# Kernel tuning notes

Hardware: AMD Instinct MI355X
Metric: run time of the kernel (lower is better)

The kernel has to match this reference:

```python
import jax, jax.numpy as jnp
import numpy as np

B, N, C, H = 4, 4096, 512, 16  # batch, seq (=input_resolution), dim, num_heads


def setup_inputs() -> dict:
    key = jax.random.key(0)
    k1, k2, k3, k4 = jax.random.split(key, 4)
    x = jax.random.normal(k1, (B, N, C), jnp.float32)
    Wqk = jax.random.normal(k2, (C, 2 * C), jnp.float32) / np.sqrt(C)
    bqk = jnp.zeros((2 * C,), jnp.float32)
    lepe_w = jax.random.normal(k3, (C, 1, 3), jnp.float32) * 0.1  # depthwise conv, groups=C
    lepe_b = jnp.zeros((C,), jnp.float32)
    return {"x": x, "Wqk": Wqk, "bqk": bqk, "lepe_w": lepe_w, "lepe_b": lepe_b}


def _rope(x):
    # x: [b, n, c]; 1D RoPE over the sequence axis, k_max = c // 2 pairs.
    b, n, c = x.shape
    k_max = c // 2
    theta = 1.0 / (10000.0 ** (jnp.arange(k_max, dtype=jnp.float32) / k_max))
    ang = jnp.arange(n, dtype=jnp.float32)[:, None] * theta  # [n, k_max]
    cos, sin = jnp.cos(ang), jnp.sin(ang)
    xr, xi = x[..., 0::2], x[..., 1::2]  # consecutive (re, im) pairs
    out = jnp.stack([xr * cos - xi * sin, xr * sin + xi * cos], axis=-1)
    return out.reshape(b, n, c)


def reference(x, Wqk, bqk, lepe_w, lepe_b):
    b, n, c = x.shape
    h = H
    d = c // h
    qk = x @ Wqk + bqk  # [b, n, 2c]
    q = jax.nn.elu(qk[..., :c]) + 1.0
    k = jax.nn.elu(qk[..., c:]) + 1.0
    q_rope = _rope(q).reshape(b, n, h, d).transpose(0, 2, 1, 3)  # [b,h,n,d]
    k_rope = _rope(k).reshape(b, n, h, d).transpose(0, 2, 1, 3)
    qh = q.reshape(b, n, h, d).transpose(0, 2, 1, 3)
    kh = k.reshape(b, n, h, d).transpose(0, 2, 1, 3)
    v = x.reshape(b, n, h, d).transpose(0, 2, 1, 3)
    # normalizer z = 1 / (q . mean_n(k) + eps)
    kmean = kh.mean(axis=2)  # [b,h,d]
    z = 1.0 / (jnp.einsum('bhnd,bhd->bhn', qh, kmean) + 1e-6)  # [b,h,n]
    # kv = (k_rope^T / sqrt(n)) @ (v / sqrt(n))
    kv = jnp.einsum('bhnd,bhne->bhde', k_rope, v) / n  # [b,h,d,d]
    out = jnp.einsum('bhnd,bhde->bhne', q_rope, kv) * z[..., None]  # [b,h,n,d]
    out = out.transpose(0, 2, 1, 3).reshape(b, n, c)
    # LePE: depthwise conv1d over sequence on v (v reassembled == x)
    vt = x.transpose(0, 2, 1)  # [b, c, n]
    lepe = jax.lax.conv_general_dilated(
        vt, lepe_w, window_strides=(1,), padding=((1, 1),),
        feature_group_count=c, dimension_numbers=('NCH', 'OIH', 'NCH'))
    lepe = lepe + lepe_b[None, :, None]
    return out + lepe.transpose(0, 2, 1)
```

## Files before the change

kernel.cpp:

```cpp
#include <hip/hip_runtime.h>

typedef unsigned short u16;
typedef u16   u16x8 __attribute__((ext_vector_type(8)));
typedef short s16x8 __attribute__((ext_vector_type(8)));
typedef float f32x4 __attribute__((ext_vector_type(4)));

__device__ __forceinline__ float b2f(u16 u) {
    return __uint_as_float(((unsigned)u) << 16);
}
__device__ __forceinline__ u16 f2b(float f) {
    unsigned x = __float_as_uint(f);
    x += 0x7fffu + ((x >> 16) & 1u);
    return (u16)(x >> 16);
}
__device__ __forceinline__ void gload_lds(const u16* g, u16* l) {
    __builtin_amdgcn_global_load_lds(
        (const __attribute__((address_space(1))) unsigned int*)g,
        (__attribute__((address_space(3))) unsigned int*)l, 16, 0, 0);
}

#define THETA_SCALE 0.05190512648261f

__global__ __launch_bounds__(256)
void k_prep(const float* __restrict__ X, u16* __restrict__ Xb,
            const float* __restrict__ W, u16* __restrict__ WT) {
    if (blockIdx.x < 4096) {
        size_t i = (size_t)(blockIdx.x * 256 + threadIdx.x) * 8;
        float4 a = *(const float4*)(X + i);
        float4 b = *(const float4*)(X + i + 4);
        u16x8 r;
        r[0] = f2b(a.x); r[1] = f2b(a.y); r[2] = f2b(a.z); r[3] = f2b(a.w);
        r[4] = f2b(b.x); r[5] = f2b(b.y); r[6] = f2b(b.z); r[7] = f2b(b.w);
        *(u16x8*)(Xb + i) = r;
    } else {
        __shared__ float tile[32][33];
        int bid = blockIdx.x - 4096;
        int c0 = (bid & 31) * 32;
        int r0 = (bid >> 5) * 32;
        int tx = threadIdx.x & 31;
        int ty = threadIdx.x >> 5;
        #pragma unroll
        for (int i = 0; i < 4; ++i) {
            int r = ty + i * 8;
            tile[r][tx] = W[(size_t)(r0 + r) * 1024 + c0 + tx];
        }
        __syncthreads();
        #pragma unroll
        for (int i = 0; i < 4; ++i) {
            int r = ty + i * 8;
            WT[(size_t)(c0 + r) * 512 + r0 + tx] = f2b(tile[tx][r]);
        }
    }
}

__global__ __launch_bounds__(256)
void k_gemm(const u16* __restrict__ Xb, const u16* __restrict__ WT,
            const float* __restrict__ bqk,
            u16* __restrict__ Qb, u16* __restrict__ Kb) {
    __shared__ u16 As[128 * 64];
    __shared__ u16 Bs[128 * 64];
    const int t = threadIdx.x;
    const int m0 = blockIdx.x * 128;
    const int n0 = blockIdx.y * 128;
    const int lane = t & 63;
    const int wave = t >> 6;
    const int wm = (wave >> 1) * 64;
    const int wn = (wave & 1) * 64;
    const int quad = lane >> 4;
    const int l16 = lane & 15;
    const int lr = lane >> 3;
    const int cg = ((lane & 7) ^ lr) * 8;

    f32x4 acc[4][4];
    f32x4 zero4 = {0.f, 0.f, 0.f, 0.f};
    #pragma unroll
    for (int i = 0; i < 4; ++i)
        #pragma unroll
        for (int j = 0; j < 4; ++j) acc[i][j] = zero4;

    for (int k0 = 0; k0 < 512; k0 += 64) {
        __syncthreads();
        #pragma unroll
        for (int g = 0; g < 4; ++g) {
            int r0 = wave * 32 + g * 8;
            size_t ga = (size_t)(m0 + r0 + lr) * 512 + k0 + cg;
            size_t gb = (size_t)(n0 + r0 + lr) * 512 + k0 + cg;
            gload_lds(Xb + ga, &As[r0 * 64]);
            gload_lds(WT + gb, &Bs[r0 * 64]);
        }
        __syncthreads();
        #pragma unroll
        for (int ks = 0; ks < 64; ks += 32) {
            const int cbase = quad + (ks >> 3);
            s16x8 a4[4], b4[4];
            #pragma unroll
            for (int i = 0; i < 4; ++i) {
                int row = wm + i * 16 + l16;
                a4[i] = *(const s16x8*)&As[row * 64 + ((cbase ^ (row & 7)) * 8)];
            }
            #pragma unroll
            for (int j = 0; j < 4; ++j) {
                int row = wn + j * 16 + l16;
                b4[j] = *(const s16x8*)&Bs[row * 64 + ((cbase ^ (row & 7)) * 8)];
            }
            #pragma unroll
            for (int i = 0; i < 4; ++i)
                #pragma unroll
                for (int j = 0; j < 4; ++j)
                    acc[i][j] = __builtin_amdgcn_mfma_f32_16x16x32_bf16(
                        a4[i], b4[j], acc[i][j], 0, 0, 0);
        }
    }

    u16* O = (n0 < 512) ? Qb : Kb;
    #pragma unroll
    for (int i = 0; i < 4; ++i)
        #pragma unroll
        for (int j = 0; j < 4; ++j) {
            int col = n0 + wn + j * 16 + l16;
            float bias = bqk[col];
            int gc = col & 511;
            #pragma unroll
            for (int r = 0; r < 4; ++r) {
                int grow = m0 + wm + i * 16 + quad * 4 + r;
                float v = acc[i][j][r] + bias;
                v = v > 0.f ? v + 1.f : __expf(v);
                O[(size_t)grow * 512 + gc] = f2b(v);
            }
        }
}

__global__ __launch_bounds__(256)
void k_kv(const u16* __restrict__ Kb, const u16* __restrict__ Xb,
          float* __restrict__ kvbuf, float* __restrict__ ksum) {
    const int bh = blockIdx.x;
    const int b = bh >> 4, h = bh & 15;
    const int nb = blockIdx.y * 512;
    __shared__ float krT_s[32 * 68];
    __shared__ float v_s[64 * 36];
    __shared__ float red_s[256 * 16];
    const int t = threadIdx.x;
    const int row = t >> 2;
    const int c8 = (t & 3) * 8;
    const int d0 = (t & 15) * 2;
    const int e0 = ((t >> 4) & 3) * 8;
    const int rg = (t >> 6) * 16;
    float ksl[8] = {0, 0, 0, 0, 0, 0, 0, 0};
    float a0[8] = {0, 0, 0, 0, 0, 0, 0, 0};
    float a1[8] = {0, 0, 0, 0, 0, 0, 0, 0};

    float th[4];
    #pragma unroll
    for (int p = 0; p < 4; ++p)
        th[p] = exp2f(-THETA_SCALE * (float)(h * 16 + (c8 >> 1) + p));

    for (int pass = 0; pass < 8; ++pass) {
        int n = nb + pass * 64 + row;
        size_t base = (size_t)(b * 4096 + n) * 512 + h * 32 + c8;
        u16x8 k8 = *(const u16x8*)(Kb + base);
        u16x8 v8 = *(const u16x8*)(Xb + base);
        float kf[8], vf[8], kr[8];
        #pragma unroll
        for (int j = 0; j < 8; ++j) { kf[j] = b2f(k8[j]); vf[j] = b2f(v8[j]); }
        #pragma unroll
        for (int p = 0; p < 4; ++p) {
            float sv, cv;
            sincosf((float)n * th[p], &sv, &cv);
            kr[2 * p]     = kf[2 * p] * cv - kf[2 * p + 1] * sv;
            kr[2 * p + 1] = kf[2 * p] * sv + kf[2 * p + 1] * cv;
        }
        #pragma unroll
        for (int j = 0; j < 8; ++j) ksl[j] += kf[j];
        if (pass) __syncthreads();
        #pragma unroll
        for (int j = 0; j < 8; ++j) krT_s[(c8 + j) * 68 + row] = kr[j];
        *(float4*)&v_s[row * 36 + c8]     = make_float4(vf[0], vf[1], vf[2], vf[3]);
        *(float4*)&v_s[row * 36 + c8 + 4] = make_float4(vf[4], vf[5], vf[6], vf[7]);
        __syncthreads();
        #pragma unroll
        for (int r = 0; r < 16; r += 4) {
            int rr0 = rg + r;
            float4 k0 = *(const float4*)&krT_s[d0 * 68 + rr0];
            float4 k1 = *(const float4*)&krT_s[(d0 + 1) * 68 + rr0];
            #pragma unroll
            for (int rr = 0; rr < 4; ++rr) {
                float4 va = *(const float4*)&v_s[(rr0 + rr) * 36 + e0];
                float4 vb = *(const float4*)&v_s[(rr0 + rr) * 36 + e0 + 4];
                float kq0 = (rr == 0) ? k0.x : (rr == 1) ? k0.y : (rr == 2) ? k0.z : k0.w;
                float kq1 = (rr == 0) ? k1.x : (rr == 1) ? k1.y : (rr == 2) ? k1.z : k1.w;
                a0[0] += kq0 * va.x; a0[1] += kq0 * va.y; a0[2] += kq0 * va.z; a0[3] += kq0 * va.w;
                a0[4] += kq0 * vb.x; a0[5] += kq0 * vb.y; a0[6] += kq0 * vb.z; a0[7] += kq0 * vb.w;
                a1[0] += kq1 * va.x; a1[1] += kq1 * va.y; a1[2] += kq1 * va.z; a1[3] += kq1 * va.w;
                a1[4] += kq1 * vb.x; a1[5] += kq1 * vb.y; a1[6] += kq1 * vb.z; a1[7] += kq1 * vb.w;
            }
        }
    }
    __syncthreads();
    #pragma unroll
    for (int j = 0; j < 8; ++j) {
        red_s[t * 16 + j] = a0[j];
        red_s[t * 16 + 8 + j] = a1[j];
    }
    __syncthreads();
    if (t < 64) {
        #pragma unroll
        for (int i = 0; i < 16; ++i) {
            float s = red_s[t * 16 + i] + red_s[(t + 64) * 16 + i] +
                      red_s[(t + 128) * 16 + i] + red_s[(t + 192) * 16 + i];
            int dd = (t & 15) * 2 + (i >> 3);
            int ee = ((t >> 4) & 3) * 8 + (i & 7);
            atomicAdd(&kvbuf[(size_t)bh * 1024 + dd * 32 + ee], s);
        }
    }
    __syncthreads();
    #pragma unroll
    for (int j = 0; j < 8; ++j) red_s[row * 32 + c8 + j] = ksl[j];
    __syncthreads();
    if (t < 32) {
        float s = 0.f;
        for (int r = 0; r < 64; ++r) s += red_s[r * 32 + t];
        atomicAdd(&ksum[bh * 32 + t], s);
    }
}

__global__ __launch_bounds__(256)
void k_out(const u16* __restrict__ Qb, const u16* __restrict__ Xb,
           const float* __restrict__ kvbuf, const float* __restrict__ ksum,
           const float* __restrict__ lw, const float* __restrict__ lb,
           float* __restrict__ OUT) {
    const int b = blockIdx.x >> 6;
    const int nb = (blockIdx.x & 63) * 64;
    const int hbase = blockIdx.y * 4;
    __shared__ float kv_s[32 * 36];
    __shared__ float qr_s[64 * 36];
    __shared__ float ks_s[32];
    __shared__ float z_s[64];
    const int t = threadIdx.x;
    const int row = t >> 2;
    const int c4 = t & 3;
    const int e0 = c4 * 8;
    const float invN = 1.f / 4096.f;
    const int n = nb + row;
    const size_t rowbase = (size_t)(b * 4096 + n) * 512;

    for (int hh = 0; hh < 4; ++hh) {
        const int h = hbase + hh;
        const int bh = b * 16 + h;
        if (hh) __syncthreads();
        #pragma unroll
        for (int i = 0; i < 4; ++i) {
            int id = t + i * 256;
            kv_s[(id >> 5) * 36 + (id & 31)] = kvbuf[(size_t)bh * 1024 + id] * invN;
        }
        if (t < 32) ks_s[t] = ksum[bh * 32 + t] * invN;
        __syncthreads();

        u16x8 q8 = *(const u16x8*)(Qb + rowbase + h * 32 + e0);
        float qf[8];
        #pragma unroll
        for (int j = 0; j < 8; ++j) qf[j] = b2f(q8[j]);
        float part = 0.f;
        #pragma unroll
        for (int j = 0; j < 8; ++j) part += qf[j] * ks_s[e0 + j];
        float qr[8];
        #pragma unroll
        for (int p = 0; p < 4; ++p) {
            float th = exp2f(-THETA_SCALE * (float)(h * 16 + c4 * 4 + p));
            float sv, cv;
            sincosf((float)n * th, &sv, &cv);
            qr[2 * p]     = qf[2 * p] * cv - qf[2 * p + 1] * sv;
            qr[2 * p + 1] = qf[2 * p] * sv + qf[2 * p + 1] * cv;
        }
        *(float4*)&qr_s[row * 36 + e0]     = make_float4(qr[0], qr[1], qr[2], qr[3]);
        *(float4*)&qr_s[row * 36 + e0 + 4] = make_float4(qr[4], qr[5], qr[6], qr[7]);
        part += __shfl_xor(part, 1);
        part += __shfl_xor(part, 2);
        if (c4 == 0) z_s[row] = 1.f / (part + 1e-6f);
        __syncthreads();

        float o[8] = {0, 0, 0, 0, 0, 0, 0, 0};
        #pragma unroll 4
        for (int dd = 0; dd < 32; ++dd) {
            float qd = qr_s[row * 36 + dd];
            const float4 k0v = *(const float4*)&kv_s[dd * 36 + e0];
            const float4 k1v = *(const float4*)&kv_s[dd * 36 + e0 + 4];
            o[0] += qd * k0v.x; o[1] += qd * k0v.y; o[2] += qd * k0v.z; o[3] += qd * k0v.w;
            o[4] += qd * k1v.x; o[5] += qd * k1v.y; o[6] += qd * k1v.z; o[7] += qd * k1v.w;
        }
        const float z = z_s[row];

        const int cb = h * 32 + e0;
        u16x8 xc = *(const u16x8*)(Xb + rowbase + cb);
        u16x8 xm = {0, 0, 0, 0, 0, 0, 0, 0};
        u16x8 xp = {0, 0, 0, 0, 0, 0, 0, 0};
        if (n > 0)    xm = *(const u16x8*)(Xb + rowbase - 512 + cb);
        if (n < 4095) xp = *(const u16x8*)(Xb + rowbase + 512 + cb);
        float rv[8];
        #pragma unroll
        for (int j = 0; j < 8; ++j) {
            int c = cb + j;
            float lep = b2f(xm[j]) * lw[c * 3] +
                        b2f(xc[j]) * lw[c * 3 + 1] +
                        b2f(xp[j]) * lw[c * 3 + 2] + lb[c];
            rv[j] = o[j] * z + lep;
        }
        float* Of = OUT + rowbase + cb;
        *(float4*)Of       = make_float4(rv[0], rv[1], rv[2], rv[3]);
        *(float4*)(Of + 4) = make_float4(rv[4], rv[5], rv[6], rv[7]);
    }
}

extern "C" void kernel_launch(void* const* d_in, const int* in_sizes, int n_in,
                              void* d_out, int out_size, void* d_ws, size_t ws_size,
                              hipStream_t stream) {
    const float* x   = (const float*)d_in[0];
    const float* Wqk = (const float*)d_in[1];
    const float* bqk = (const float*)d_in[2];
    const float* lw  = (const float*)d_in[3];
    const float* lb  = (const float*)d_in[4];
    float* out = (float*)d_out;

    char* w = (char*)d_ws;
    u16* Kb      = (u16*)w;   w += (size_t)16384 * 512 * 2;
    u16* Qb      = (u16*)w;   w += (size_t)16384 * 512 * 2;
    u16* Xb      = (u16*)w;   w += (size_t)16384 * 512 * 2;
    u16* WT      = (u16*)w;   w += (size_t)1024 * 512 * 2;
    float* kvbuf = (float*)w; w += (size_t)64 * 1024 * 4;
    float* ksum  = (float*)w;

    hipMemsetAsync(kvbuf, 0, (size_t)64 * 1024 * 4 + (size_t)64 * 32 * 4, stream);
    k_prep<<<4608, 256, 0, stream>>>(x, Xb, Wqk, WT);
    k_gemm<<<dim3(128, 8), 256, 0, stream>>>(Xb, WT, bqk, Qb, Kb);
    k_kv<<<dim3(64, 8), 256, 0, stream>>>(Kb, Xb, kvbuf, ksum);
    k_out<<<dim3(256, 4), 256, 0, stream>>>(Qb, Xb, kvbuf, ksum, lw, lb, out);
}
```

Measured before the change: 168.4 us.

## Use bf16 MFMA for kv accumulation and fold buffer zeroing into prep kernel

The k_v/k_rope outer-product reduction now stages rotated K and V transposed in swizzled bf16 LDS tiles and accumulates with 16x16x32 bf16 MFMA instructions. This replaces the scalar FP32 FMA loop and the shared-memory cross-thread reduction. The separate memset of the kv and ksum accumulators is replaced by extra blocks in the prep kernel, saving one launch. Rounding rotated K to bf16 adds some precision loss.

```diff
diff --git a/kernel.cpp b/kernel.cpp
--- a/kernel.cpp
+++ b/kernel.cpp
@@ -23,7 +23,8 @@
 
 __global__ __launch_bounds__(256)
 void k_prep(const float* __restrict__ X, u16* __restrict__ Xb,
-            const float* __restrict__ W, u16* __restrict__ WT) {
+            const float* __restrict__ W, u16* __restrict__ WT,
+            float* __restrict__ kvz) {
     if (blockIdx.x < 4096) {
         size_t i = (size_t)(blockIdx.x * 256 + threadIdx.x) * 8;
         float4 a = *(const float4*)(X + i);
@@ -32,7 +33,7 @@
         r[0] = f2b(a.x); r[1] = f2b(a.y); r[2] = f2b(a.z); r[3] = f2b(a.w);
         r[4] = f2b(b.x); r[5] = f2b(b.y); r[6] = f2b(b.z); r[7] = f2b(b.w);
         *(u16x8*)(Xb + i) = r;
-    } else {
+    } else if (blockIdx.x < 4608) {
         __shared__ float tile[32][33];
         int bid = blockIdx.x - 4096;
         int c0 = (bid & 31) * 32;
@@ -50,6 +51,9 @@
             int r = ty + i * 8;
             WT[(size_t)(c0 + r) * 512 + r0 + tx] = f2b(tile[tx][r]);
         }
+    } else {
+        size_t i = (size_t)(blockIdx.x - 4608) * 1024 + threadIdx.x * 4;
+        *(float4*)(kvz + i) = make_float4(0.f, 0.f, 0.f, 0.f);
     }
 }
 
@@ -136,18 +140,26 @@
     const int bh = blockIdx.x;
     const int b = bh >> 4, h = bh & 15;
     const int nb = blockIdx.y * 512;
-    __shared__ float krT_s[32 * 68];
-    __shared__ float v_s[64 * 36];
-    __shared__ float red_s[256 * 16];
+    __shared__ u16 krT[32 * 72];
+    __shared__ u16 vT[32 * 72];
+    __shared__ float red[64 * 36];
     const int t = threadIdx.x;
     const int row = t >> 2;
     const int c8 = (t & 3) * 8;
-    const int d0 = (t & 15) * 2;
-    const int e0 = ((t >> 4) & 3) * 8;
-    const int rg = (t >> 6) * 16;
+    const int rot_w = 16 * ((c8 >> 3) & 3);
+    const int lane = t & 63;
+    const int wave = t >> 6;
+    const int quad = lane >> 4;
+    const int l16 = lane & 15;
+    const int dq = (wave >> 1) * 16;
+    const int eq = (wave & 1) * 16;
+    const int ca = dq + l16;
+    const int cb2 = eq + l16;
+    const int rot_a = 16 * ((ca >> 3) & 3);
+    const int rot_b = 16 * ((cb2 >> 3) & 3);
+
     float ksl[8] = {0, 0, 0, 0, 0, 0, 0, 0};
-    float a0[8] = {0, 0, 0, 0, 0, 0, 0, 0};
-    float a1[8] = {0, 0, 0, 0, 0, 0, 0, 0};
+    f32x4 acc = {0.f, 0.f, 0.f, 0.f};
 
     float th[4];
     #pragma unroll
@@ -159,9 +171,9 @@
         size_t base = (size_t)(b * 4096 + n) * 512 + h * 32 + c8;
         u16x8 k8 = *(const u16x8*)(Kb + base);
         u16x8 v8 = *(const u16x8*)(Xb + base);
-        float kf[8], vf[8], kr[8];
-        #pragma unroll
-        for (int j = 0; j < 8; ++j) { kf[j] = b2f(k8[j]); vf[j] = b2f(v8[j]); }
+        float kf[8], kr[8];
+        #pragma unroll
+        for (int j = 0; j < 8; ++j) kf[j] = b2f(k8[j]);
         #pragma unroll
         for (int p = 0; p < 4; ++p) {
             float sv, cv;
@@ -172,53 +184,33 @@
         #pragma unroll
         for (int j = 0; j < 8; ++j) ksl[j] += kf[j];
         if (pass) __syncthreads();
-        #pragma unroll
-        for (int j = 0; j < 8; ++j) krT_s[(c8 + j) * 68 + row] = kr[j];
-        *(float4*)&v_s[row * 36 + c8]     = make_float4(vf[0], vf[1], vf[2], vf[3]);
-        *(float4*)&v_s[row * 36 + c8 + 4] = make_float4(vf[4], vf[5], vf[6], vf[7]);
-        __syncthreads();
-        #pragma unroll
-        for (int r = 0; r < 16; r += 4) {
-            int rr0 = rg + r;
-            float4 k0 = *(const float4*)&krT_s[d0 * 68 + rr0];
-            float4 k1 = *(const float4*)&krT_s[(d0 + 1) * 68 + rr0];
-            #pragma unroll
-            for (int rr = 0; rr < 4; ++rr) {
-                float4 va = *(const float4*)&v_s[(rr0 + rr) * 36 + e0];
-                float4 vb = *(const float4*)&v_s[(rr0 + rr) * 36 + e0 + 4];
-                float kq0 = (rr == 0) ? k0.x : (rr == 1) ? k0.y : (rr == 2) ? k0.z : k0.w;
-                float kq1 = (rr == 0) ? k1.x : (rr == 1) ? k1.y : (rr == 2) ? k1.z : k1.w;
-                a0[0] += kq0 * va.x; a0[1] += kq0 * va.y; a0[2] += kq0 * va.z; a0[3] += kq0 * va.w;
-                a0[4] += kq0 * vb.x; a0[5] += kq0 * vb.y; a0[6] += kq0 * vb.z; a0[7] += kq0 * vb.w;
-                a1[0] += kq1 * va.x; a1[1] += kq1 * va.y; a1[2] += kq1 * va.z; a1[3] += kq1 * va.w;
-                a1[4] += kq1 * vb.x; a1[5] += kq1 * vb.y; a1[6] += kq1 * vb.z; a1[7] += kq1 * vb.w;
-            }
-        }
-    }
+        int colw = (row + rot_w) & 63;
+        #pragma unroll
+        for (int j = 0; j < 8; ++j) {
+            krT[(c8 + j) * 72 + colw] = f2b(kr[j]);
+            vT[(c8 + j) * 72 + colw] = v8[j];
+        }
+        __syncthreads();
+        #pragma unroll
+        for (int ks = 0; ks < 64; ks += 32) {
+            s16x8 a4 = *(const s16x8*)&krT[ca * 72 + ((ks + quad * 8 + rot_a) & 63)];
+            s16x8 b4 = *(const s16x8*)&vT[cb2 * 72 + ((ks + quad * 8 + rot_b) & 63)];
+            acc = __builtin_amdgcn_mfma_f32_16x16x32_bf16(a4, b4, acc, 0, 0, 0);
+        }
+    }
+
+    #pragma unroll
+    for (int r = 0; r < 4; ++r)
+        atomicAdd(&kvbuf[(size_t)bh * 1024 + (dq + quad * 4 + r) * 32 + eq + l16],
+                  acc[r]);
+
     __syncthreads();
-    #pragma unroll
-    for (int j = 0; j < 8; ++j) {
-        red_s[t * 16 + j] = a0[j];
-        red_s[t * 16 + 8 + j] = a1[j];
-    }
-    __syncthreads();
-    if (t < 64) {
-        #pragma unroll
-        for (int i = 0; i < 16; ++i) {
-            float s = red_s[t * 16 + i] + red_s[(t + 64) * 16 + i] +
-                      red_s[(t + 128) * 16 + i] + red_s[(t + 192) * 16 + i];
-            int dd = (t & 15) * 2 + (i >> 3);
-            int ee = ((t >> 4) & 3) * 8 + (i & 7);
-            atomicAdd(&kvbuf[(size_t)bh * 1024 + dd * 32 + ee], s);
-        }
-    }
-    __syncthreads();
-    #pragma unroll
-    for (int j = 0; j < 8; ++j) red_s[row * 32 + c8 + j] = ksl[j];
+    *(float4*)&red[row * 36 + c8]     = make_float4(ksl[0], ksl[1], ksl[2], ksl[3]);
+    *(float4*)&red[row * 36 + c8 + 4] = make_float4(ksl[4], ksl[5], ksl[6], ksl[7]);
     __syncthreads();
     if (t < 32) {
         float s = 0.f;
-        for (int r = 0; r < 64; ++r) s += red_s[r * 32 + t];
+        for (int r = 0; r < 64; ++r) s += red[r * 36 + t];
         atomicAdd(&ksum[bh * 32 + t], s);
     }
 }
@@ -328,8 +320,7 @@
     float* kvbuf = (float*)w; w += (size_t)64 * 1024 * 4;
     float* ksum  = (float*)w;
 
-    hipMemsetAsync(kvbuf, 0, (size_t)64 * 1024 * 4 + (size_t)64 * 32 * 4, stream);
-    k_prep<<<4608, 256, 0, stream>>>(x, Xb, Wqk, WT);
+    k_prep<<<4674, 256, 0, stream>>>(x, Xb, Wqk, WT, kvbuf);
     k_gemm<<<dim3(128, 8), 256, 0, stream>>>(Xb, WT, bqk, Qb, Kb);
     k_kv<<<dim3(64, 8), 256, 0, stream>>>(Kb, Xb, kvbuf, ksum);
     k_out<<<dim3(256, 4), 256, 0, stream>>>(Qb, Xb, kvbuf, ksum, lw, lb, out);
```

Measured after the change: 147.9 us. 12.1% less time.
